# Kernel tuning notes

Measured on AMD Instinct MI355X. Metric: run time of the kernel, lower is better.

Reference implementation:

```python
import jax, jax.numpy as jnp
import numpy as np

NUM_USERS = 100000
NUM_JOBS = 50000
NUM_EDGES = 2000000
NUM_LABELS = 500000
HID = 128
USER_DIM = 512
JOB_DIM = 768
BN_EPS = 1e-5


def setup_inputs() -> dict:
    key = jax.random.key(0)
    ks = iter(jax.random.split(key, 40))
    d = {}
    d['user_x'] = jax.random.normal(next(ks), (NUM_USERS, USER_DIM), jnp.float32)
    d['job_x'] = jax.random.normal(next(ks), (NUM_JOBS, JOB_DIM), jnp.float32)
    d['user_W'] = jax.random.normal(next(ks), (HID, USER_DIM), jnp.float32) * 0.05
    d['user_b'] = jax.random.normal(next(ks), (HID,), jnp.float32)
    d['user_gamma'] = jax.random.uniform(next(ks), (HID,), jnp.float32)
    d['user_beta'] = jax.random.normal(next(ks), (HID,), jnp.float32)
    d['user_mean'] = jax.random.normal(next(ks), (HID,), jnp.float32)
    d['user_var'] = jax.random.uniform(next(ks), (HID,), jnp.float32)
    d['job_W'] = jax.random.normal(next(ks), (HID, JOB_DIM), jnp.float32) * 0.05
    d['job_b'] = jax.random.normal(next(ks), (HID,), jnp.float32)
    d['job_gamma'] = jax.random.uniform(next(ks), (HID,), jnp.float32)
    d['job_beta'] = jax.random.normal(next(ks), (HID,), jnp.float32)
    d['job_mean'] = jax.random.normal(next(ks), (HID,), jnp.float32)
    d['job_var'] = jax.random.uniform(next(ks), (HID,), jnp.float32)
    for nm in ['l1_rates_Wl', 'l1_rates_Wr', 'l1_rev_Wl', 'l1_rev_Wr',
               'l2_rates_Wl', 'l2_rates_Wr', 'l2_rev_Wl', 'l2_rev_Wr']:
        d[nm] = jax.random.normal(next(ks), (HID, HID), jnp.float32) * 0.08
    for nm in ['l1_rates_bl', 'l1_rev_bl', 'l2_rates_bl', 'l2_rev_bl']:
        d[nm] = jax.random.normal(next(ks), (HID,), jnp.float32) * 0.05
    d['rates_src'] = jax.random.randint(next(ks), (NUM_EDGES,), 0, NUM_USERS, jnp.int64 if jax.config.jax_enable_x64 else jnp.int32)
    d['rates_dst'] = jax.random.randint(next(ks), (NUM_EDGES,), 0, NUM_JOBS, jnp.int32)
    d['label_src'] = jax.random.randint(next(ks), (NUM_LABELS,), 0, NUM_USERS, jnp.int32)
    d['label_dst'] = jax.random.randint(next(ks), (NUM_LABELS,), 0, NUM_JOBS, jnp.int32)
    return d


def _mean_aggr(x_src, src_idx, dst_idx, num_dst):
    # scatter-mean of gathered source features onto destination nodes
    s = jax.ops.segment_sum(x_src[src_idx], dst_idx, num_segments=num_dst)
    cnt = jax.ops.segment_sum(jnp.ones(src_idx.shape[0], x_src.dtype), dst_idx, num_segments=num_dst)
    return s / jnp.maximum(cnt, 1.0)[:, None]


def _sage(x_src, x_dst, src_idx, dst_idx, Wl, bl, Wr):
    agg = _mean_aggr(x_src, src_idx, dst_idx, x_dst.shape[0])
    return agg @ Wl.T + bl + x_dst @ Wr.T


def _bn(x, gamma, beta, mean, var):
    return (x - mean) * (gamma * jax.lax.rsqrt(var + BN_EPS)) + beta


def reference(user_x, job_x, user_W, user_b, user_gamma, user_beta, user_mean, user_var,
              job_W, job_b, job_gamma, job_beta, job_mean, job_var,
              l1_rates_Wl, l1_rates_bl, l1_rates_Wr, l1_rev_Wl, l1_rev_bl, l1_rev_Wr,
              l2_rates_Wl, l2_rates_bl, l2_rates_Wr, l2_rev_Wl, l2_rev_bl, l2_rev_Wr,
              rates_src, rates_dst, label_src, label_dst):
    # node-type encoders: Linear -> BN(eval) -> ReLU  (dropout is identity in eval)
    u = jax.nn.relu(_bn(user_x @ user_W.T + user_b, user_gamma, user_beta, user_mean, user_var))
    j = jax.nn.relu(_bn(job_x @ job_W.T + job_b, job_gamma, job_beta, job_mean, job_var))
    # hetero SAGE layer 1: rates (user->job), rev_rates (job->user)
    j1 = jax.nn.relu(_sage(u, j, rates_src, rates_dst, l1_rates_Wl, l1_rates_bl, l1_rates_Wr))
    u1 = jax.nn.relu(_sage(j, u, rates_dst, rates_src, l1_rev_Wl, l1_rev_bl, l1_rev_Wr))
    # hetero SAGE layer 2 (no activation after, matches GNN.forward)
    j2 = _sage(u1, j1, rates_src, rates_dst, l2_rates_Wl, l2_rates_bl, l2_rates_Wr)
    u2 = _sage(j1, u1, rates_dst, rates_src, l2_rev_Wl, l2_rev_bl, l2_rev_Wr)
    # dot-product link classifier over label edges
    return jnp.sum(u2[label_src] * j2[label_dst], axis=1)
```

## Files before the change

kernel.cpp:

```cpp
#include <hip/hip_runtime.h>
#include <cstdint>
#include <cstddef>

#define HID 128
#define N_USERS 100000
#define N_JOBS  50000
#define N_EDGES 2000000
#define N_LABELS 500000

#define RBITS 8
#define RSIZE 256
#define NBJ ((N_JOBS  + RSIZE - 1) / RSIZE)
#define NBU ((N_USERS + RSIZE - 1) / RSIZE)
#define P1CHUNK 8192

typedef __attribute__((ext_vector_type(8))) short short8;
typedef __attribute__((ext_vector_type(4))) float f32x4;

__device__ __forceinline__ unsigned short f2b(float f) {
    union { float f; unsigned u; } v; v.f = f;
    unsigned r = v.u + 0x7FFFu + ((v.u >> 16) & 1u);
    return (unsigned short)(r >> 16);
}
__device__ __forceinline__ float b2f(unsigned h) {
    union { unsigned u; float f; } v; v.u = h << 16;
    return v.f;
}
__device__ __forceinline__ unsigned pk2(float lo, float hi) {
    return (unsigned)f2b(lo) | ((unsigned)f2b(hi) << 16);
}
__device__ __forceinline__ void gl_lds16(const void* g, void* l) {
    __builtin_amdgcn_global_load_lds(
        (const __attribute__((address_space(1))) unsigned int*)g,
        (__attribute__((address_space(3))) unsigned int*)l, 16, 0, 0);
}

__global__ __launch_bounds__(256) void cvt_weights(
    const float* __restrict__ uW, const float* __restrict__ jW,
    const float* __restrict__ a, const float* __restrict__ b,
    const float* __restrict__ c, const float* __restrict__ d,
    const float* __restrict__ e, const float* __restrict__ f,
    const float* __restrict__ g, const float* __restrict__ h,
    unsigned short* __restrict__ ow) {
    int i4 = blockIdx.x * 256 + threadIdx.x;
    if (i4 >= 73728) return;
    int i = i4 * 4;
    const float* src; int base;
    if (i < 65536)       { src = uW; base = 0; }
    else if (i < 163840) { src = jW; base = 65536; }
    else {
        int k = (i - 163840) >> 14;
        const float* s4 = (k < 4) ? ((k < 2) ? (k == 0 ? a : b) : (k == 2 ? c : d))
                                  : ((k < 6) ? (k == 4 ? e : f) : (k == 6 ? g : h));
        src = s4; base = 163840 + (k << 14);
    }
    float4 v = *reinterpret_cast<const float4*>(src + (i - base));
    *reinterpret_cast<uint2*>(ow + i) = make_uint2(pk2(v.x, v.y), pk2(v.z, v.w));
}

__global__ __launch_bounds__(256) void bucket_hist(const int* __restrict__ src,
                                                   const int* __restrict__ dst,
                                                   int nE, int* __restrict__ bcnt_j,
                                                   int* __restrict__ bcnt_u) {
    __shared__ int hj[NBJ];
    __shared__ int hu[NBU];
    int t = threadIdx.x;
    for (int i = t; i < NBJ; i += 256) hj[i] = 0;
    for (int i = t; i < NBU; i += 256) hu[i] = 0;
    __syncthreads();
    int i = blockIdx.x * blockDim.x + t;
    int stride = gridDim.x * blockDim.x;
    for (; i < nE; i += stride) {
        atomicAdd(&hj[dst[i] >> RBITS], 1);
        atomicAdd(&hu[src[i] >> RBITS], 1);
    }
    __syncthreads();
    for (int i2 = t; i2 < NBJ; i2 += 256) if (hj[i2]) atomicAdd(&bcnt_j[i2], hj[i2]);
    for (int i2 = t; i2 < NBU; i2 += 256) if (hu[i2]) atomicAdd(&bcnt_u[i2], hu[i2]);
}

__global__ __launch_bounds__(1024) void bucket_scan(int* __restrict__ bcnt_j, int* __restrict__ boff_j,
                                                    int* __restrict__ bcur_j,
                                                    int* __restrict__ bcnt_u, int* __restrict__ boff_u,
                                                    int* __restrict__ bcur_u) {
    int* bcnt = blockIdx.x ? bcnt_u : bcnt_j;
    int* boff = blockIdx.x ? boff_u : boff_j;
    int* bcur = blockIdx.x ? bcur_u : bcur_j;
    int n = blockIdx.x ? NBU : NBJ;
    __shared__ int sm[1024];
    int t = threadIdx.x;
    int v = (t < n) ? bcnt[t] : 0;
    sm[t] = v;
    __syncthreads();
    for (int d = 1; d < 1024; d <<= 1) {
        int q = (t >= d) ? sm[t - d] : 0;
        __syncthreads();
        sm[t] += q;
        __syncthreads();
    }
    if (t < n) { int e = sm[t] - v; boff[t] = e; bcur[t] = e; }
    if (t == 0) boff[n] = N_EDGES;
}

__global__ __launch_bounds__(256) void csr_pass1(const int* __restrict__ src,
                                                 const int* __restrict__ dst,
                                                 int nE, int* __restrict__ gcur_j,
                                                 int* __restrict__ gcur_u,
                                                 unsigned* __restrict__ stage_j,
                                                 unsigned* __restrict__ stage_u) {
    __shared__ int cur_j[NBJ];
    __shared__ int cur_u[NBU];
    int t = threadIdx.x;
    int e0 = blockIdx.x * P1CHUNK;
    int e1 = min(e0 + P1CHUNK, nE);
    for (int i = t; i < NBJ; i += 256) cur_j[i] = 0;
    for (int i = t; i < NBU; i += 256) cur_u[i] = 0;
    __syncthreads();
    for (int e = e0 + t; e < e1; e += 256) {
        atomicAdd(&cur_j[dst[e] >> RBITS], 1);
        atomicAdd(&cur_u[src[e] >> RBITS], 1);
    }
    __syncthreads();
    for (int i = t; i < NBJ; i += 256) {
        int c = cur_j[i];
        cur_j[i] = c ? atomicAdd(&gcur_j[i], c) : 0;
    }
    for (int i = t; i < NBU; i += 256) {
        int c = cur_u[i];
        cur_u[i] = c ? atomicAdd(&gcur_u[i], c) : 0;
    }
    __syncthreads();
    for (int e = e0 + t; e < e1; e += 256) {
        int d = dst[e], s = src[e];
        int pj = atomicAdd(&cur_j[d >> RBITS], 1);
        stage_j[pj] = ((unsigned)(d & (RSIZE - 1)) << 24) | (unsigned)s;
        int pu = atomicAdd(&cur_u[s >> RBITS], 1);
        stage_u[pu] = ((unsigned)(s & (RSIZE - 1)) << 24) | (unsigned)d;
    }
}

__global__ __launch_bounds__(256) void csr_pass2(
    const unsigned* __restrict__ stage_j, const int* __restrict__ boff_j,
    int* __restrict__ off_j, int* __restrict__ vals_j,
    const unsigned* __restrict__ stage_u, const int* __restrict__ boff_u,
    int* __restrict__ off_u, int* __restrict__ vals_u) {
    __shared__ int cnt[RSIZE];
    __shared__ int sc[RSIZE];
    __shared__ int cur[RSIZE];
    int borig = blockIdx.x, t = threadIdx.x;
    const unsigned* words; const int* boff; int* off; int* vals; int b; int nNodes;
    if (borig < NBJ) { words = stage_j; boff = boff_j; off = off_j; vals = vals_j; b = borig; nNodes = N_JOBS; }
    else             { words = stage_u; boff = boff_u; off = off_u; vals = vals_u; b = borig - NBJ; nNodes = N_USERS; }
    int node0 = b << RBITS;
    int sbeg = boff[b], send = boff[b + 1];
    cnt[t] = 0;
    __syncthreads();
    for (int e = sbeg + t; e < send; e += 256) {
        atomicAdd(&cnt[words[e] >> 24], 1);
    }
    __syncthreads();
    int v = cnt[t];
    sc[t] = v;
    __syncthreads();
    #pragma unroll
    for (int d = 1; d < RSIZE; d <<= 1) {
        int q = (t >= d) ? sc[t - d] : 0;
        __syncthreads();
        sc[t] += q;
        __syncthreads();
    }
    int node = node0 + t;
    if (node < nNodes) {
        int base = sbeg + sc[t] - v;
        off[node] = base;
        cur[t] = base;
    }
    __syncthreads();
    for (int e = sbeg + t; e < send; e += 256) {
        unsigned w = words[e];
        int slot = atomicAdd(&cur[w >> 24], 1);
        vals[slot] = (int)(w & 0xFFFFFFu);
    }
    if (t == 0 && borig == 0)   off_j[N_JOBS]  = N_EDGES;
    if (t == 0 && borig == NBJ) off_u[N_USERS] = N_EDGES;
}

__global__ __launch_bounds__(256) void aggregate_bf16(const unsigned short* __restrict__ x,
                                                      const int* __restrict__ off,
                                                      const int* __restrict__ vals,
                                                      unsigned short* __restrict__ out, int nDst) {
    int node = blockIdx.x * 4 + (threadIdx.x >> 6);
    if (node >= nDst) return;
    int lane = threadIdx.x & 63;
    int beg = off[node], end = off[node + 1];
    float a0 = 0.f, a1 = 0.f;
    int e = beg;
    for (; e + 3 < end; e += 4) {
        int s0 = vals[e], s1 = vals[e + 1], s2 = vals[e + 2], s3 = vals[e + 3];
        unsigned v0 = *reinterpret_cast<const unsigned*>(x + (size_t)s0 * HID + lane * 2);
        unsigned v1 = *reinterpret_cast<const unsigned*>(x + (size_t)s1 * HID + lane * 2);
        unsigned v2 = *reinterpret_cast<const unsigned*>(x + (size_t)s2 * HID + lane * 2);
        unsigned v3 = *reinterpret_cast<const unsigned*>(x + (size_t)s3 * HID + lane * 2);
        a0 += b2f(v0 & 0xffffu) + b2f(v1 & 0xffffu) + b2f(v2 & 0xffffu) + b2f(v3 & 0xffffu);
        a1 += b2f(v0 >> 16) + b2f(v1 >> 16) + b2f(v2 >> 16) + b2f(v3 >> 16);
    }
    for (; e < end; ++e) {
        unsigned v0 = *reinterpret_cast<const unsigned*>(x + (size_t)vals[e] * HID + lane * 2);
        a0 += b2f(v0 & 0xffffu);
        a1 += b2f(v0 >> 16);
    }
    float inv = 1.0f / fmaxf((float)(end - beg), 1.0f);
    unsigned r = (unsigned)f2b(a0 * inv) | ((unsigned)f2b(a1 * inv) << 16);
    *reinterpret_cast<unsigned*>(out + (size_t)node * HID + lane * 2) = r;
}

__global__ __launch_bounds__(256) void encoder_mfma(
    const float* __restrict__ X, const unsigned short* __restrict__ Wb,
    const float* __restrict__ bias, const float* __restrict__ gamma,
    const float* __restrict__ beta, const float* __restrict__ mean,
    const float* __restrict__ var, unsigned short* __restrict__ out, int M, int K) {
    __shared__ float lds[2][4096];
    int tid = threadIdx.x;
    int m0 = blockIdx.x * 64;
    int w = tid >> 6, lane = tid & 63;
    int lrow = lane & 15, lgrp = lane >> 4;
    f32x4 acc[4][2];
    #pragma unroll
    for (int m = 0; m < 4; ++m)
        #pragma unroll
        for (int n = 0; n < 2; ++n) acc[m][n] = (f32x4){0.f, 0.f, 0.f, 0.f};

    const unsigned short* wp[2];
    #pragma unroll
    for (int n = 0; n < 2; ++n)
        wp[n] = Wb + (size_t)(w * 32 + n * 16 + lrow) * K + lgrp * 8;

    auto STAGE = [&](int t, int b) {
        int k0 = t << 6;
        #pragma unroll
        for (int c = 0; c < 4; ++c) {
            int unit = c * 256 + tid;
            int row = unit >> 4, u = unit & 15;
            int gr = m0 + row; if (gr > M - 1) gr = M - 1;
            const float* g = X + (size_t)gr * K + k0 + ((u ^ (row & 15)) << 2);
            gl_lds16(g, (void*)&lds[b][unit * 4]);
        }
    };
    auto LOADW = [&](int t, short8* dst) {
        int k0 = t << 6;
        #pragma unroll
        for (int ks = 0; ks < 2; ++ks)
            #pragma unroll
            for (int n = 0; n < 2; ++n)
                dst[ks * 2 + n] = *reinterpret_cast<const short8*>(wp[n] + k0 + ks * 32);
    };

    int nt = K >> 6;
    short8 bfc[4], bfn[4];
    LOADW(0, bfc);
    STAGE(0, 0);
    __syncthreads();
    for (int t = 0; t < nt; ++t) {
        if (t + 1 < nt) { LOADW(t + 1, bfn); STAGE(t + 1, (t + 1) & 1); }
        const float* bufp = &lds[t & 1][0];
        #pragma unroll
        for (int ks = 0; ks < 2; ++ks) {
            int p = ks * 4 + lgrp;
            #pragma unroll
            for (int m = 0; m < 4; ++m) {
                int row = m * 16 + lrow;
                int swz = row & 15;
                float4 ra = *reinterpret_cast<const float4*>(bufp + row * 64 + (((2 * p)     ^ swz) << 2));
                float4 rb = *reinterpret_cast<const float4*>(bufp + row * 64 + (((2 * p + 1) ^ swz) << 2));
                union { unsigned u[4]; short8 s; } r;
                r.u[0] = pk2(ra.x, ra.y); r.u[1] = pk2(ra.z, ra.w);
                r.u[2] = pk2(rb.x, rb.y); r.u[3] = pk2(rb.z, rb.w);
                acc[m][0] = __builtin_amdgcn_mfma_f32_16x16x32_bf16(bfc[ks * 2 + 0], r.s, acc[m][0], 0, 0, 0);
                acc[m][1] = __builtin_amdgcn_mfma_f32_16x16x32_bf16(bfc[ks * 2 + 1], r.s, acc[m][1], 0, 0, 0);
            }
        }
        __syncthreads();
        if (t + 1 < nt) {
            #pragma unroll
            for (int i = 0; i < 4; ++i) bfc[i] = bfn[i];
        }
    }

    float sc[2][4], sh[2][4];
    #pragma unroll
    for (int n = 0; n < 2; ++n)
        #pragma unroll
        for (int j = 0; j < 4; ++j) {
            int gc = w * 32 + n * 16 + lgrp * 4 + j;
            float s = gamma[gc] * rsqrtf(var[gc] + 1e-5f);
            sc[n][j] = s;
            sh[n][j] = (bias[gc] - mean[gc]) * s + beta[gc];
        }
    #pragma unroll
    for (int m = 0; m < 4; ++m) {
        int row = m0 + m * 16 + lrow;
        if (row < M) {
            #pragma unroll
            for (int n = 0; n < 2; ++n) {
                float v0 = fmaxf(acc[m][n][0] * sc[n][0] + sh[n][0], 0.f);
                float v1 = fmaxf(acc[m][n][1] * sc[n][1] + sh[n][1], 0.f);
                float v2 = fmaxf(acc[m][n][2] * sc[n][2] + sh[n][2], 0.f);
                float v3 = fmaxf(acc[m][n][3] * sc[n][3] + sh[n][3], 0.f);
                *reinterpret_cast<uint2*>(out + (size_t)row * HID + w * 32 + n * 16 + lgrp * 4) =
                    make_uint2(pk2(v0, v1), pk2(v2, v3));
            }
        }
    }
}

__global__ __launch_bounds__(256) void sage_mfma(
    const unsigned short* __restrict__ Aagg, const unsigned short* __restrict__ Bx,
    const unsigned short* __restrict__ WA, const unsigned short* __restrict__ WB,
    const float* __restrict__ bl, void* __restrict__ outv,
    int M, int doRelu, int outF32) {
    __shared__ unsigned short lds[2][4096];
    int tid = threadIdx.x;
    int m0 = blockIdx.x * 64;
    int w = tid >> 6, lane = tid & 63;
    int lrow = lane & 15, lgrp = lane >> 4;
    f32x4 acc[4][2];
    #pragma unroll
    for (int m = 0; m < 4; ++m)
        #pragma unroll
        for (int n = 0; n < 2; ++n) acc[m][n] = (f32x4){0.f, 0.f, 0.f, 0.f};

    auto STAGE = [&](int s, int b) {
        const unsigned short* Ap = (s < 2) ? Aagg : Bx;
        int k0 = (s & 1) << 6;
        #pragma unroll
        for (int c = 0; c < 2; ++c) {
            int unit = c * 256 + tid;
            int row = unit >> 3, u = unit & 7;
            int gr = m0 + row; if (gr > M - 1) gr = M - 1;
            const unsigned short* g = Ap + (size_t)gr * HID + k0 + ((u ^ (row & 7)) << 3);
            gl_lds16(g, (void*)&lds[b][unit * 8]);
        }
    };
    auto LOADW = [&](int s, short8* dst) {
        const unsigned short* Wp = (s < 2) ? WA : WB;
        int k0 = (s & 1) << 6;
        #pragma unroll
        for (int ks = 0; ks < 2; ++ks)
            #pragma unroll
            for (int n = 0; n < 2; ++n)
                dst[ks * 2 + n] = *reinterpret_cast<const short8*>(
                    Wp + (size_t)(w * 32 + n * 16 + lrow) * HID + k0 + ks * 32 + lgrp * 8);
    };

    short8 bfc[4], bfn[4];
    LOADW(0, bfc);
    STAGE(0, 0);
    __syncthreads();
    #pragma unroll
    for (int s = 0; s < 4; ++s) {
        if (s < 3) { LOADW(s + 1, bfn); STAGE(s + 1, (s + 1) & 1); }
        const unsigned short* bufp = &lds[s & 1][0];
        #pragma unroll
        for (int ks = 0; ks < 2; ++ks) {
            int p = ks * 4 + lgrp;
            #pragma unroll
            for (int m = 0; m < 4; ++m) {
                int row = m * 16 + lrow;
                short8 af = *reinterpret_cast<const short8*>(bufp + row * 64 + ((p ^ (row & 7)) << 3));
                acc[m][0] = __builtin_amdgcn_mfma_f32_16x16x32_bf16(bfc[ks * 2 + 0], af, acc[m][0], 0, 0, 0);
                acc[m][1] = __builtin_amdgcn_mfma_f32_16x16x32_bf16(bfc[ks * 2 + 1], af, acc[m][1], 0, 0, 0);
            }
        }
        __syncthreads();
        if (s < 3) {
            #pragma unroll
            for (int i = 0; i < 4; ++i) bfc[i] = bfn[i];
        }
    }

    float blv[2][4];
    #pragma unroll
    for (int n = 0; n < 2; ++n)
        #pragma unroll
        for (int j = 0; j < 4; ++j)
            blv[n][j] = bl[w * 32 + n * 16 + lgrp * 4 + j];
    #pragma unroll
    for (int m = 0; m < 4; ++m) {
        int row = m0 + m * 16 + lrow;
        if (row < M) {
            #pragma unroll
            for (int n = 0; n < 2; ++n) {
                float v[4];
                #pragma unroll
                for (int j = 0; j < 4; ++j) {
                    float x = acc[m][n][j] + blv[n][j];
                    v[j] = doRelu ? fmaxf(x, 0.f) : x;
                }
                int col0 = w * 32 + n * 16 + lgrp * 4;
                if (outF32) {
                    *reinterpret_cast<float4*>((float*)outv + (size_t)row * HID + col0) =
                        make_float4(v[0], v[1], v[2], v[3]);
                } else {
                    *reinterpret_cast<uint2*>((unsigned short*)outv + (size_t)row * HID + col0) =
                        make_uint2(pk2(v[0], v[1]), pk2(v[2], v[3]));
                }
            }
        }
    }
}

__global__ __launch_bounds__(256) void dot_kernel(const float* __restrict__ U,
                                                  const float* __restrict__ J,
                                                  const int* __restrict__ ls,
                                                  const int* __restrict__ ld,
                                                  float* __restrict__ out, int nL) {
    int gw = (int)((blockIdx.x * blockDim.x + threadIdx.x) >> 5);
    int l = threadIdx.x & 31;
    if (gw >= nL) return;
    int a = ls[gw], c = ld[gw];
    float4 uv = *reinterpret_cast<const float4*>(U + (size_t)a * HID + l * 4);
    float4 jv = *reinterpret_cast<const float4*>(J + (size_t)c * HID + l * 4);
    float p = uv.x * jv.x + uv.y * jv.y + uv.z * jv.z + uv.w * jv.w;
    #pragma unroll
    for (int s = 16; s > 0; s >>= 1) p += __shfl_xor(p, s, 64);
    if (l == 0) out[gw] = p;
}

extern "C" void kernel_launch(void* const* d_in, const int* in_sizes, int n_in,
                              void* d_out, int out_size, void* d_ws, size_t ws_size,
                              hipStream_t stream) {
    const float* user_x     = (const float*)d_in[0];
    const float* job_x      = (const float*)d_in[1];
    const float* user_W     = (const float*)d_in[2];
    const float* user_b     = (const float*)d_in[3];
    const float* user_gamma = (const float*)d_in[4];
    const float* user_beta  = (const float*)d_in[5];
    const float* user_mean  = (const float*)d_in[6];
    const float* user_var   = (const float*)d_in[7];
    const float* job_W      = (const float*)d_in[8];
    const float* job_b      = (const float*)d_in[9];
    const float* job_gamma  = (const float*)d_in[10];
    const float* job_beta   = (const float*)d_in[11];
    const float* job_mean   = (const float*)d_in[12];
    const float* job_var    = (const float*)d_in[13];
    const float* l1_rates_Wl = (const float*)d_in[14];
    const float* l1_rates_Wr = (const float*)d_in[15];
    const float* l1_rev_Wl   = (const float*)d_in[16];
    const float* l1_rev_Wr   = (const float*)d_in[17];
    const float* l2_rates_Wl = (const float*)d_in[18];
    const float* l2_rates_Wr = (const float*)d_in[19];
    const float* l2_rev_Wl   = (const float*)d_in[20];
    const float* l2_rev_Wr   = (const float*)d_in[21];
    const float* l1_rates_bl = (const float*)d_in[22];
    const float* l1_rev_bl   = (const float*)d_in[23];
    const float* l2_rates_bl = (const float*)d_in[24];
    const float* l2_rev_bl   = (const float*)d_in[25];
    const int* rates_src = (const int*)d_in[26];
    const int* rates_dst = (const int*)d_in[27];
    const int* label_src = (const int*)d_in[28];
    const int* label_dst = (const int*)d_in[29];

    char* ws = (char*)d_ws;
    size_t o = 0;
    auto alloc = [&](size_t bytes) -> void* {
        void* p = ws + o;
        o = (o + bytes + 511) & ~(size_t)511;
        return p;
    };
    unsigned short* u_bf = (unsigned short*)alloc((size_t)N_USERS * HID * 2);
    unsigned short* j_bf = (unsigned short*)alloc((size_t)N_JOBS  * HID * 2);
    unsigned short* u1   = (unsigned short*)alloc((size_t)N_USERS * HID * 2);
    unsigned short* j1   = (unsigned short*)alloc((size_t)N_JOBS  * HID * 2);
    unsigned short* aggU = (unsigned short*)alloc((size_t)N_USERS * HID * 2);
    unsigned short* aggJ = (unsigned short*)alloc((size_t)N_JOBS  * HID * 2);
    float* u2f = (float*)alloc((size_t)N_USERS * HID * 4);
    float* j2f = (float*)alloc((size_t)N_JOBS  * HID * 4);
    int* vals_j = (int*)alloc((size_t)N_EDGES * 4);
    int* vals_u = (int*)alloc((size_t)N_EDGES * 4);
    unsigned* stage_j = (unsigned*)alloc((size_t)N_EDGES * 4);
    unsigned* stage_u = (unsigned*)alloc((size_t)N_EDGES * 4);
    int* off_j  = (int*)alloc((size_t)(N_JOBS + 1) * 4);
    int* off_u  = (int*)alloc((size_t)(N_USERS + 1) * 4);
    int* bcnt_j = (int*)alloc((size_t)(NBJ + 1) * 4);
    int* bcnt_u = (int*)alloc((size_t)(NBU + 1) * 4);
    int* boff_j = (int*)alloc((size_t)(NBJ + 1) * 4);
    int* boff_u = (int*)alloc((size_t)(NBU + 1) * 4);
    int* bcur_j = (int*)alloc((size_t)(NBJ + 1) * 4);
    int* bcur_u = (int*)alloc((size_t)(NBU + 1) * 4);
    unsigned short* wbf = (unsigned short*)alloc((size_t)294912 * 2);
    (void)ws_size; (void)n_in; (void)in_sizes; (void)out_size;

    const unsigned short* uWb = wbf;
    const unsigned short* jWb = wbf + 65536;
    const unsigned short* w8  = wbf + 163840;

    cvt_weights<<<288, 256, 0, stream>>>(user_W, job_W,
        l1_rates_Wl, l1_rates_Wr, l1_rev_Wl, l1_rev_Wr,
        l2_rates_Wl, l2_rates_Wr, l2_rev_Wl, l2_rev_Wr, wbf);

    hipMemsetAsync(bcnt_j, 0, (size_t)(NBJ + 1) * 4, stream);
    hipMemsetAsync(bcnt_u, 0, (size_t)(NBU + 1) * 4, stream);
    bucket_hist<<<512, 256, 0, stream>>>(rates_src, rates_dst, N_EDGES, bcnt_j, bcnt_u);
    bucket_scan<<<2, 1024, 0, stream>>>(bcnt_j, boff_j, bcur_j, bcnt_u, boff_u, bcur_u);
    csr_pass1<<<(N_EDGES + P1CHUNK - 1) / P1CHUNK, 256, 0, stream>>>(
        rates_src, rates_dst, N_EDGES, bcur_j, bcur_u, stage_j, stage_u);
    csr_pass2<<<NBJ + NBU, 256, 0, stream>>>(stage_j, boff_j, off_j, vals_j,
                                             stage_u, boff_u, off_u, vals_u);

    encoder_mfma<<<(N_USERS + 63) / 64, 256, 0, stream>>>(
        user_x, uWb, user_b, user_gamma, user_beta, user_mean, user_var, u_bf, N_USERS, 512);
    encoder_mfma<<<(N_JOBS + 63) / 64, 256, 0, stream>>>(
        job_x, jWb, job_b, job_gamma, job_beta, job_mean, job_var, j_bf, N_JOBS, 768);

    aggregate_bf16<<<(N_JOBS + 3) / 4, 256, 0, stream>>>(u_bf, off_j, vals_j, aggJ, N_JOBS);
    sage_mfma<<<(N_JOBS + 63) / 64, 256, 0, stream>>>(
        aggJ, j_bf, w8 + 0 * 16384, w8 + 1 * 16384, l1_rates_bl, (void*)j1, N_JOBS, 1, 0);
    aggregate_bf16<<<(N_USERS + 3) / 4, 256, 0, stream>>>(j_bf, off_u, vals_u, aggU, N_USERS);
    sage_mfma<<<(N_USERS + 63) / 64, 256, 0, stream>>>(
        aggU, u_bf, w8 + 2 * 16384, w8 + 3 * 16384, l1_rev_bl, (void*)u1, N_USERS, 1, 0);

    aggregate_bf16<<<(N_JOBS + 3) / 4, 256, 0, stream>>>(u1, off_j, vals_j, aggJ, N_JOBS);
    sage_mfma<<<(N_JOBS + 63) / 64, 256, 0, stream>>>(
        aggJ, j1, w8 + 4 * 16384, w8 + 5 * 16384, l2_rates_bl, (void*)j2f, N_JOBS, 0, 1);
    aggregate_bf16<<<(N_USERS + 3) / 4, 256, 0, stream>>>(j1, off_u, vals_u, aggU, N_USERS);
    sage_mfma<<<(N_USERS + 63) / 64, 256, 0, stream>>>(
        aggU, u1, w8 + 6 * 16384, w8 + 7 * 16384, l2_rev_bl, (void*)u2f, N_USERS, 0, 1);

    dot_kernel<<<(N_LABELS * 32 + 255) / 256, 256, 0, stream>>>(
        u2f, j2f, label_src, label_dst, (float*)d_out, N_LABELS);
}
```

Before: 686.3 us.

## Merge user/job launches per stage, split aggregation lanes, store layer-2 outputs as bf16

```diff
diff --git a/kernel.cpp b/kernel.cpp
--- a/kernel.cpp
+++ b/kernel.cpp
@@ -13,6 +13,11 @@
 #define NBJ ((N_JOBS  + RSIZE - 1) / RSIZE)
 #define NBU ((N_USERS + RSIZE - 1) / RSIZE)
 #define P1CHUNK 8192
+
+#define TBU ((N_USERS + 63) / 64)
+#define TBJ ((N_JOBS  + 63) / 64)
+#define ABJ ((N_JOBS  + 3) / 4)
+#define ABU ((N_USERS + 3) / 4)
 
 typedef __attribute__((ext_vector_type(8))) short short8;
 typedef __attribute__((ext_vector_type(4))) float f32x4;
@@ -185,43 +190,77 @@
     if (t == 0 && borig == NBJ) off_u[N_USERS] = N_EDGES;
 }
 
-__global__ __launch_bounds__(256) void aggregate_bf16(const unsigned short* __restrict__ x,
-                                                      const int* __restrict__ off,
-                                                      const int* __restrict__ vals,
-                                                      unsigned short* __restrict__ out, int nDst) {
-    int node = blockIdx.x * 4 + (threadIdx.x >> 6);
+__global__ __launch_bounds__(256) void aggregate2(
+    const unsigned short* __restrict__ xJ, const int* __restrict__ offJ,
+    const int* __restrict__ valsJ, unsigned short* __restrict__ outJ,
+    const unsigned short* __restrict__ xU, const int* __restrict__ offU,
+    const int* __restrict__ valsU, unsigned short* __restrict__ outU) {
+    int bb = blockIdx.x;
+    const unsigned short* x; const int* off; const int* vals; unsigned short* out;
+    int nDst, node0;
+    if (bb < ABJ) { x = xJ; off = offJ; vals = valsJ; out = outJ; nDst = N_JOBS;  node0 = bb * 4; }
+    else          { x = xU; off = offU; vals = valsU; out = outU; nDst = N_USERS; node0 = (bb - ABJ) * 4; }
+    int node = node0 + (threadIdx.x >> 6);
     if (node >= nDst) return;
     int lane = threadIdx.x & 63;
+    int hl = lane & 31;
+    int eo = lane >> 5;
     int beg = off[node], end = off[node + 1];
-    float a0 = 0.f, a1 = 0.f;
+    float a0 = 0.f, a1 = 0.f, a2 = 0.f, a3 = 0.f;
     int e = beg;
     for (; e + 3 < end; e += 4) {
-        int s0 = vals[e], s1 = vals[e + 1], s2 = vals[e + 2], s3 = vals[e + 3];
-        unsigned v0 = *reinterpret_cast<const unsigned*>(x + (size_t)s0 * HID + lane * 2);
-        unsigned v1 = *reinterpret_cast<const unsigned*>(x + (size_t)s1 * HID + lane * 2);
-        unsigned v2 = *reinterpret_cast<const unsigned*>(x + (size_t)s2 * HID + lane * 2);
-        unsigned v3 = *reinterpret_cast<const unsigned*>(x + (size_t)s3 * HID + lane * 2);
-        a0 += b2f(v0 & 0xffffu) + b2f(v1 & 0xffffu) + b2f(v2 & 0xffffu) + b2f(v3 & 0xffffu);
-        a1 += b2f(v0 >> 16) + b2f(v1 >> 16) + b2f(v2 >> 16) + b2f(v3 >> 16);
-    }
-    for (; e < end; ++e) {
-        unsigned v0 = *reinterpret_cast<const unsigned*>(x + (size_t)vals[e] * HID + lane * 2);
-        a0 += b2f(v0 & 0xffffu);
-        a1 += b2f(v0 >> 16);
-    }
-    float inv = 1.0f / fmaxf((float)(end - beg), 1.0f);
-    unsigned r = (unsigned)f2b(a0 * inv) | ((unsigned)f2b(a1 * inv) << 16);
-    *reinterpret_cast<unsigned*>(out + (size_t)node * HID + lane * 2) = r;
+        int s0 = vals[e + eo], s1 = vals[e + 2 + eo];
+        uint2 v0 = *reinterpret_cast<const uint2*>(x + (size_t)s0 * HID + hl * 4);
+        uint2 v1 = *reinterpret_cast<const uint2*>(x + (size_t)s1 * HID + hl * 4);
+        a0 += b2f(v0.x & 0xffffu) + b2f(v1.x & 0xffffu);
+        a1 += b2f(v0.x >> 16)     + b2f(v1.x >> 16);
+        a2 += b2f(v0.y & 0xffffu) + b2f(v1.y & 0xffffu);
+        a3 += b2f(v0.y >> 16)     + b2f(v1.y >> 16);
+    }
+    for (; e < end; e += 2) {
+        int ee = e + eo;
+        if (ee < end) {
+            int s = vals[ee];
+            uint2 v = *reinterpret_cast<const uint2*>(x + (size_t)s * HID + hl * 4);
+            a0 += b2f(v.x & 0xffffu);
+            a1 += b2f(v.x >> 16);
+            a2 += b2f(v.y & 0xffffu);
+            a3 += b2f(v.y >> 16);
+        }
+    }
+    a0 += __shfl_xor(a0, 32, 64);
+    a1 += __shfl_xor(a1, 32, 64);
+    a2 += __shfl_xor(a2, 32, 64);
+    a3 += __shfl_xor(a3, 32, 64);
+    if (eo == 0) {
+        float inv = 1.0f / fmaxf((float)(end - beg), 1.0f);
+        *reinterpret_cast<uint2*>(out + (size_t)node * HID + hl * 4) =
+            make_uint2(pk2(a0 * inv, a1 * inv), pk2(a2 * inv, a3 * inv));
+    }
 }
 
 __global__ __launch_bounds__(256) void encoder_mfma(
-    const float* __restrict__ X, const unsigned short* __restrict__ Wb,
-    const float* __restrict__ bias, const float* __restrict__ gamma,
-    const float* __restrict__ beta, const float* __restrict__ mean,
-    const float* __restrict__ var, unsigned short* __restrict__ out, int M, int K) {
+    const float* __restrict__ Xu, const unsigned short* __restrict__ Wbu,
+    const float* __restrict__ bu, const float* __restrict__ gu,
+    const float* __restrict__ beu, const float* __restrict__ mu,
+    const float* __restrict__ vu,
+    const float* __restrict__ Xj, const unsigned short* __restrict__ Wbj,
+    const float* __restrict__ bj, const float* __restrict__ gj,
+    const float* __restrict__ bej, const float* __restrict__ mj,
+    const float* __restrict__ vj,
+    unsigned short* __restrict__ outU, unsigned short* __restrict__ outJ) {
     __shared__ float lds[2][4096];
+    const float *X, *bias, *gamma, *beta, *mean, *var;
+    const unsigned short* Wb; unsigned short* out;
+    int M, K, m0;
+    if (blockIdx.x < TBU) {
+        X = Xu; Wb = Wbu; bias = bu; gamma = gu; beta = beu; mean = mu; var = vu;
+        out = outU; M = N_USERS; K = 512; m0 = blockIdx.x * 64;
+    } else {
+        X = Xj; Wb = Wbj; bias = bj; gamma = gj; beta = bej; mean = mj; var = vj;
+        out = outJ; M = N_JOBS; K = 768; m0 = (blockIdx.x - TBU) * 64;
+    }
     int tid = threadIdx.x;
-    int m0 = blockIdx.x * 64;
     int w = tid >> 6, lane = tid & 63;
     int lrow = lane & 15, lgrp = lane >> 4;
     f32x4 acc[4][2];
@@ -314,13 +353,24 @@
 }
 
 __global__ __launch_bounds__(256) void sage_mfma(
-    const unsigned short* __restrict__ Aagg, const unsigned short* __restrict__ Bx,
-    const unsigned short* __restrict__ WA, const unsigned short* __restrict__ WB,
-    const float* __restrict__ bl, void* __restrict__ outv,
-    int M, int doRelu, int outF32) {
+    const unsigned short* __restrict__ AaggJ, const unsigned short* __restrict__ BxJ,
+    const unsigned short* __restrict__ WAj, const unsigned short* __restrict__ WBj,
+    const float* __restrict__ blJ, unsigned short* __restrict__ outJ,
+    const unsigned short* __restrict__ AaggU, const unsigned short* __restrict__ BxU,
+    const unsigned short* __restrict__ WAu, const unsigned short* __restrict__ WBu,
+    const float* __restrict__ blU, unsigned short* __restrict__ outU,
+    int doRelu) {
     __shared__ unsigned short lds[2][4096];
+    const unsigned short *Aagg, *Bx, *WA, *WB; const float* bl; unsigned short* out;
+    int M, m0;
+    if (blockIdx.x < TBJ) {
+        Aagg = AaggJ; Bx = BxJ; WA = WAj; WB = WBj; bl = blJ; out = outJ;
+        M = N_JOBS; m0 = blockIdx.x * 64;
+    } else {
+        Aagg = AaggU; Bx = BxU; WA = WAu; WB = WBu; bl = blU; out = outU;
+        M = N_USERS; m0 = (blockIdx.x - TBJ) * 64;
+    }
     int tid = threadIdx.x;
-    int m0 = blockIdx.x * 64;
     int w = tid >> 6, lane = tid & 63;
     int lrow = lane & 15, lgrp = lane >> 4;
     f32x4 acc[4][2];
@@ -396,34 +446,31 @@
                     float x = acc[m][n][j] + blv[n][j];
                     v[j] = doRelu ? fmaxf(x, 0.f) : x;
                 }
-                int col0 = w * 32 + n * 16 + lgrp * 4;
-                if (outF32) {
-                    *reinterpret_cast<float4*>((float*)outv + (size_t)row * HID + col0) =
-                        make_float4(v[0], v[1], v[2], v[3]);
-                } else {
-                    *reinterpret_cast<uint2*>((unsigned short*)outv + (size_t)row * HID + col0) =
-                        make_uint2(pk2(v[0], v[1]), pk2(v[2], v[3]));
-                }
+                *reinterpret_cast<uint2*>(out + (size_t)row * HID + w * 32 + n * 16 + lgrp * 4) =
+                    make_uint2(pk2(v[0], v[1]), pk2(v[2], v[3]));
             }
         }
     }
 }
 
-__global__ __launch_bounds__(256) void dot_kernel(const float* __restrict__ U,
-                                                  const float* __restrict__ J,
+__global__ __launch_bounds__(256) void dot_kernel(const unsigned short* __restrict__ U,
+                                                  const unsigned short* __restrict__ J,
                                                   const int* __restrict__ ls,
                                                   const int* __restrict__ ld,
                                                   float* __restrict__ out, int nL) {
-    int gw = (int)((blockIdx.x * blockDim.x + threadIdx.x) >> 5);
-    int l = threadIdx.x & 31;
-    if (gw >= nL) return;
-    int a = ls[gw], c = ld[gw];
-    float4 uv = *reinterpret_cast<const float4*>(U + (size_t)a * HID + l * 4);
-    float4 jv = *reinterpret_cast<const float4*>(J + (size_t)c * HID + l * 4);
-    float p = uv.x * jv.x + uv.y * jv.y + uv.z * jv.z + uv.w * jv.w;
+    int ew = (int)((blockIdx.x * blockDim.x + threadIdx.x) >> 5);
+    int hl = threadIdx.x & 31;
+    if (ew >= nL) return;
+    int a = ls[ew], c = ld[ew];
+    uint2 uv = *reinterpret_cast<const uint2*>(U + (size_t)a * HID + hl * 4);
+    uint2 jv = *reinterpret_cast<const uint2*>(J + (size_t)c * HID + hl * 4);
+    float p = b2f(uv.x & 0xffffu) * b2f(jv.x & 0xffffu)
+            + b2f(uv.x >> 16)     * b2f(jv.x >> 16)
+            + b2f(uv.y & 0xffffu) * b2f(jv.y & 0xffffu)
+            + b2f(uv.y >> 16)     * b2f(jv.y >> 16);
     #pragma unroll
     for (int s = 16; s > 0; s >>= 1) p += __shfl_xor(p, s, 64);
-    if (l == 0) out[gw] = p;
+    if (hl == 0) out[ew] = p;
 }
 
 extern "C" void kernel_launch(void* const* d_in, const int* in_sizes, int n_in,
@@ -473,8 +520,8 @@
     unsigned short* j1   = (unsigned short*)alloc((size_t)N_JOBS  * HID * 2);
     unsigned short* aggU = (unsigned short*)alloc((size_t)N_USERS * HID * 2);
     unsigned short* aggJ = (unsigned short*)alloc((size_t)N_JOBS  * HID * 2);
-    float* u2f = (float*)alloc((size_t)N_USERS * HID * 4);
-    float* j2f = (float*)alloc((size_t)N_JOBS  * HID * 4);
+    unsigned short* u2b  = (unsigned short*)alloc((size_t)N_USERS * HID * 2);
+    unsigned short* j2b  = (unsigned short*)alloc((size_t)N_JOBS  * HID * 2);
     int* vals_j = (int*)alloc((size_t)N_EDGES * 4);
     int* vals_u = (int*)alloc((size_t)N_EDGES * 4);
     unsigned* stage_j = (unsigned*)alloc((size_t)N_EDGES * 4);
@@ -507,25 +554,23 @@
     csr_pass2<<<NBJ + NBU, 256, 0, stream>>>(stage_j, boff_j, off_j, vals_j,
                                              stage_u, boff_u, off_u, vals_u);
 
-    encoder_mfma<<<(N_USERS + 63) / 64, 256, 0, stream>>>(
-        user_x, uWb, user_b, user_gamma, user_beta, user_mean, user_var, u_bf, N_USERS, 512);
-    encoder_mfma<<<(N_JOBS + 63) / 64, 256, 0, stream>>>(
-        job_x, jWb, job_b, job_gamma, job_beta, job_mean, job_var, j_bf, N_JOBS, 768);
-
-    aggregate_bf16<<<(N_JOBS + 3) / 4, 256, 0, stream>>>(u_bf, off_j, vals_j, aggJ, N_JOBS);
-    sage_mfma<<<(N_JOBS + 63) / 64, 256, 0, stream>>>(
-        aggJ, j_bf, w8 + 0 * 16384, w8 + 1 * 16384, l1_rates_bl, (void*)j1, N_JOBS, 1, 0);
-    aggregate_bf16<<<(N_USERS + 3) / 4, 256, 0, stream>>>(j_bf, off_u, vals_u, aggU, N_USERS);
-    sage_mfma<<<(N_USERS + 63) / 64, 256, 0, stream>>>(
-        aggU, u_bf, w8 + 2 * 16384, w8 + 3 * 16384, l1_rev_bl, (void*)u1, N_USERS, 1, 0);
-
-    aggregate_bf16<<<(N_JOBS + 3) / 4, 256, 0, stream>>>(u1, off_j, vals_j, aggJ, N_JOBS);
-    sage_mfma<<<(N_JOBS + 63) / 64, 256, 0, stream>>>(
-        aggJ, j1, w8 + 4 * 16384, w8 + 5 * 16384, l2_rates_bl, (void*)j2f, N_JOBS, 0, 1);
-    aggregate_bf16<<<(N_USERS + 3) / 4, 256, 0, stream>>>(j1, off_u, vals_u, aggU, N_USERS);
-    sage_mfma<<<(N_USERS + 63) / 64, 256, 0, stream>>>(
-        aggU, u1, w8 + 6 * 16384, w8 + 7 * 16384, l2_rev_bl, (void*)u2f, N_USERS, 0, 1);
+    encoder_mfma<<<TBU + TBJ, 256, 0, stream>>>(
+        user_x, uWb, user_b, user_gamma, user_beta, user_mean, user_var,
+        job_x, jWb, job_b, job_gamma, job_beta, job_mean, job_var,
+        u_bf, j_bf);
+
+    aggregate2<<<ABJ + ABU, 256, 0, stream>>>(u_bf, off_j, vals_j, aggJ,
+                                              j_bf, off_u, vals_u, aggU);
+    sage_mfma<<<TBJ + TBU, 256, 0, stream>>>(
+        aggJ, j_bf, w8 + 0 * 16384, w8 + 1 * 16384, l1_rates_bl, j1,
+        aggU, u_bf, w8 + 2 * 16384, w8 + 3 * 16384, l1_rev_bl,   u1, 1);
+
+    aggregate2<<<ABJ + ABU, 256, 0, stream>>>(u1, off_j, vals_j, aggJ,
+                                              j1, off_u, vals_u, aggU);
+    sage_mfma<<<TBJ + TBU, 256, 0, stream>>>(
+        aggJ, j1, w8 + 4 * 16384, w8 + 5 * 16384, l2_rates_bl, j2b,
+        aggU, u1, w8 + 6 * 16384, w8 + 7 * 16384, l2_rev_bl,   u2b, 0);
 
     dot_kernel<<<(N_LABELS * 32 + 255) / 256, 256, 0, stream>>>(
-        u2f, j2f, label_src, label_dst, (float*)d_out, N_LABELS);
-}
+        u2b, j2b, label_src, label_dst, (float*)d_out, N_LABELS);
+}
```

New measurement: 682.9 us. About the same (-0.5%).
